# Kernel optimization log

Hardware: AMD Instinct MI355X
Metric: run time of the kernel (lower is better)

Reference implementation:

```python
import jax, jax.numpy as jnp
import numpy as np

INPUT_SIZE = 32
UNITS = 1024
T = 8192
N_MODULES = 2
INPUT_SCALING = 1.0
SPECTRAL_RADIUS = 0.99
LEAKY = 0.5
C_IN = 10
C_REC = 10


def _sparse_input_kernel(rng, M, N, C):
    # each row (input dim) projects to C random reservoir units, U(-1,1)
    W = np.zeros((M, N), dtype=np.float32)
    for i in range(M):
        idx = rng.choice(N, size=C, replace=False)
        W[i, idx] = rng.uniform(-1.0, 1.0, size=C).astype(np.float32)
    return W


def _sparse_recurrent_kernel(rng, M, C):
    # each column (unit) receives input from C random units, U(-1,1)
    W = np.zeros((M, M), dtype=np.float32)
    for i in range(M):
        idx = rng.choice(M, size=C, replace=False)
        W[idx, i] = rng.uniform(-1.0, 1.0, size=C).astype(np.float32)
    return W


def _make_recurrent(rng, M, leaky, rho):
    W = _sparse_recurrent_kernel(rng, M, C_REC)
    I = np.eye(M, dtype=np.float32)
    if leaky == 1:
        e = np.linalg.eigvals(W)
        W = W * (rho / np.max(np.abs(e)))
    else:
        W = W * leaky + I * (1.0 - leaky)
        e = np.linalg.eigvals(W)
        W = W * (rho / np.max(np.abs(e)))
        W = (W + I * (leaky - 1.0)) * (1.0 / leaky)
    return W.astype(np.float32)


def setup_inputs() -> dict:
    key = jax.random.key(0)
    rng = np.random.default_rng(0)
    u = jax.random.normal(key, (1, T, INPUT_SIZE), dtype=jnp.float32)
    # module 0: input_size -> units; module 1: units -> units
    kernel0 = jnp.asarray(_sparse_input_kernel(rng, INPUT_SIZE, UNITS, C_IN) * INPUT_SCALING)
    rec0 = jnp.asarray(_make_recurrent(rng, UNITS, LEAKY, SPECTRAL_RADIUS))
    bias0 = jnp.asarray(rng.uniform(-1.0, 1.0, size=UNITS).astype(np.float32))
    kernel1 = jnp.asarray(_sparse_input_kernel(rng, UNITS, UNITS, C_IN) * INPUT_SCALING)
    rec1 = jnp.asarray(_make_recurrent(rng, UNITS, LEAKY, SPECTRAL_RADIUS))
    bias1 = jnp.asarray(rng.uniform(-1.0, 1.0, size=UNITS).astype(np.float32))
    return {"u": u, "kernel0": kernel0, "rec0": rec0, "bias0": bias0,
            "kernel1": kernel1, "rec1": rec1, "bias1": bias1}


def _run_reservoir(u, K, W, b):
    # u: [B, T, in]; leaky-integrator ESN scan over time
    def step(h, ut):
        out = jnp.tanh(ut @ K + b + h @ W)
        h_new = h * (1.0 - LEAKY) + out * LEAKY
        return h_new, h_new
    h0 = jnp.zeros((u.shape[0], K.shape[1]), dtype=u.dtype)
    _, hs = jax.lax.scan(step, h0, jnp.swapaxes(u, 0, 1))  # [T, B, units]
    return jnp.swapaxes(hs, 0, 1)  # [B, T, units]


def reference(u, kernel0, rec0, bias0, kernel1, rec1, bias1):
    hs0 = _run_reservoir(u, kernel0, rec0, bias0)
    hs1 = _run_reservoir(hs0, kernel1, rec1, bias1)
    # deep reservoir output: concatenation of all module state sequences
    return jnp.concatenate([hs0, hs1], axis=-1)  # [1, T, 2*UNITS]
```

## Files before the change

### kernel.cpp

```cpp
#include <hip/hip_runtime.h>
#include <math.h>

typedef unsigned int uint;

#define T_STEPS 8192
#define R_CAP 10
#define K1_CAP 32
#define K0_CAP 8

__global__ __launch_bounds__(256) void prep_extract(
    const float* __restrict__ k0w, const float* __restrict__ r0w,
    const float* __restrict__ r1w, const float* __restrict__ k1w,
    float* __restrict__ r0vr, uint* __restrict__ r0ur, float* __restrict__ d0r,
    float* __restrict__ r1vr, uint* __restrict__ r1ur, float* __restrict__ d1r,
    float* __restrict__ k1vr, uint* __restrict__ k1ur, int* __restrict__ c1r,
    float* __restrict__ k0vr, uint* __restrict__ k0ur, int* __restrict__ c0r)
{
    int tid = blockIdx.x * 256 + threadIdx.x;
    int task = tid >> 10, j = tid & 1023;

    if (task <= 1) {
        const float* W = task ? r1w : r0w;
        float* vr = task ? r1vr : r0vr;
        uint*  ur = task ? r1ur : r0ur;
        float* dr = task ? d1r  : d0r;
        float diag = 0.f; int c = 0;
#pragma unroll 4
        for (int i = 0; i < 1024; ++i) {
            float v = W[i * 1024 + j];
            if (i == j) diag = v;
            else if (v != 0.f && c < R_CAP) {
                vr[j * R_CAP + c] = v; ur[j * R_CAP + c] = (uint)i; ++c;
            }
        }
        for (; c < R_CAP; ++c) { vr[j * R_CAP + c] = 0.f; ur[j * R_CAP + c] = 0u; }
        dr[j] = diag;
    } else if (task == 2) {
        int c = 0;
#pragma unroll 4
        for (int i = 0; i < 1024; ++i) {
            float v = k1w[i * 1024 + j];
            if (v != 0.f && c < K1_CAP) {
                k1vr[j * K1_CAP + c] = v; k1ur[j * K1_CAP + c] = (uint)i; ++c;
            }
        }
        c1r[j] = c;
        for (int q = c; q < K1_CAP; ++q) { k1vr[j * K1_CAP + q] = 0.f; k1ur[j * K1_CAP + q] = 0u; }
    } else {
        int c = 0;
        for (int i = 0; i < 32; ++i) {
            float v = k0w[i * 1024 + j];
            if (v != 0.f && c < K0_CAP) {
                k0vr[j * K0_CAP + c] = v; k0ur[j * K0_CAP + c] = (uint)i; ++c;
            }
        }
        c0r[j] = c;
        for (int q = c; q < K0_CAP; ++q) { k0vr[j * K0_CAP + q] = 0.f; k0ur[j * K0_CAP + q] = 0u; }
    }
}

__global__ __launch_bounds__(1024) void prep_slots(
    const float* __restrict__ r0vr, const uint* __restrict__ r0ur,
    const float* __restrict__ r1vr, const uint* __restrict__ r1ur,
    const float* __restrict__ k1vr, const uint* __restrict__ k1ur, const int* __restrict__ c1r,
    const float* __restrict__ k0vr, const uint* __restrict__ k0ur, const int* __restrict__ c0r,
    uint* __restrict__ Gr0a, float* __restrict__ Gr0v, int* __restrict__ Gcr0,
    uint* __restrict__ Gr1a, float* __restrict__ Gr1v, int* __restrict__ Gcr1,
    uint* __restrict__ Gk1a, float* __restrict__ Gk1v, int* __restrict__ Fc1,
    uint* __restrict__ Gk0a, float* __restrict__ Gk0v, int* __restrict__ Fc0,
    int* __restrict__ Fu0, int* __restrict__ Fu1,
    int* __restrict__ Linv0, int* __restrict__ Linv1)
{
    __shared__ int lc1[1024], lc0[1024];
    __shared__ unsigned short sl0[1024], sl1[1024];
    const int j = threadIdx.x;
    const int c1j = c1r[j], c0j = c0r[j];
    lc1[j] = c1j; lc0[j] = c0j;
    __syncthreads();
    int s1 = 0, s0 = 0;
#pragma unroll 4
    for (int i = 0; i < 1024; ++i) {
        int a = lc1[i]; s1 += (a < c1j) || (a == c1j && i < j);
        int b = lc0[i]; s0 += (b < c0j) || (b == c0j && i < j);
    }
    sl0[j] = (unsigned short)s0;
    sl1[j] = (unsigned short)s1;
    __syncthreads();

    {
        int n = 0;
        for (int k = 0; k < R_CAP; ++k) {
            float v = r0vr[j * R_CAP + k];
            uint  u = r0ur[j * R_CAP + k];
            Gr0v[s0 * R_CAP + k] = v;
            Gr0a[s0 * R_CAP + k] = (v != 0.f) ? ((uint)sl0[u] << 2) : 0u;
            if (v != 0.f) n = k + 1;
        }
        Gcr0[s0] = n;
        for (int k = 0; k < K0_CAP; ++k) {
            Gk0v[s0 * K0_CAP + k] = k0vr[j * K0_CAP + k];
            Gk0a[s0 * K0_CAP + k] = (k < c0j) ? (k0ur[j * K0_CAP + k] << 2) : 0u;
        }
        Fc0[s0] = c0j; Fu0[s0] = j;
    }
    {
        int n = 0;
        for (int k = 0; k < R_CAP; ++k) {
            float v = r1vr[j * R_CAP + k];
            uint  u = r1ur[j * R_CAP + k];
            Gr1v[s1 * R_CAP + k] = v;
            Gr1a[s1 * R_CAP + k] = (v != 0.f) ? ((uint)sl1[u] << 2) : 0u;
            if (v != 0.f) n = k + 1;
        }
        Gcr1[s1] = n;
        for (int k = 0; k < K1_CAP; ++k) {
            Gk1v[s1 * K1_CAP + k] = k1vr[j * K1_CAP + k];
            Gk1a[s1 * K1_CAP + k] = (k < c1j) ? ((uint)sl0[k1ur[j * K1_CAP + k]] << 2) : 0u;
        }
        Fc1[s1] = c1j; Fu1[s1] = j;
    }
    Linv0[j] = s0;
    Linv1[j] = s1;
}

__global__ __launch_bounds__(256) void prep_greedy(
    const uint* __restrict__ Gr0a, const float* __restrict__ Gr0v, const int* __restrict__ Gcr0,
    const uint* __restrict__ Gr1a, const float* __restrict__ Gr1v, const int* __restrict__ Gcr1,
    const uint* __restrict__ Gk1a, const float* __restrict__ Gk1v, const int* __restrict__ Fc1,
    const uint* __restrict__ Gk0a, const float* __restrict__ Gk0v, const int* __restrict__ Fc0,
    float* __restrict__ Fr0v, uint* __restrict__ Fr0a,
    float* __restrict__ Fr1v, uint* __restrict__ Fr1a,
    float* __restrict__ Fk1v, uint* __restrict__ Fk1a,
    float* __restrict__ Fk0v, uint* __restrict__ Fk0a)
{
    __shared__ uint  ea[4][64][32];
    __shared__ float ev[4][64][32];
    __shared__ int   bl[4][32];
    const int wv   = threadIdx.x >> 6;
    const int lane = threadIdx.x & 63;
    const int gw   = blockIdx.x * 4 + wv;
    const int task = gw >> 4;
    const int col  = (gw & 15) * 64 + lane;

    const uint* ga; const float* gv; const int* gc; int cap;
    float* fv; uint* fa;
    if (task == 0)      { ga = Gr0a; gv = Gr0v; gc = Gcr0; cap = R_CAP;  fv = Fr0v; fa = Fr0a; }
    else if (task == 1) { ga = Gr1a; gv = Gr1v; gc = Gcr1; cap = R_CAP;  fv = Fr1v; fa = Fr1a; }
    else if (task == 2) { ga = Gk1a; gv = Gk1v; gc = Fc1;  cap = K1_CAP; fv = Fk1v; fa = Fk1a; }
    else                { ga = Gk0a; gv = Gk0v; gc = Fc0;  cap = K0_CAP; fv = Fk0v; fa = Fk0a; }

    const int cnt = gc[col];
    for (int s = 0; s < cap; ++s) {
        ea[wv][lane][s] = ga[col * cap + s];
        ev[wv][lane][s] = gv[col * cap + s];
    }
    __syncthreads();

    for (int slot = 0; slot < 32; ++slot) {
        if (lane < 32) bl[wv][lane] = 0;
        __syncthreads();
        int pick = -1;
        const bool active = (slot < cap) && (slot < cnt);
        for (int rnd = 0; rnd < 3; ++rnd) {
            if (active && pick < 0) {
                int best = slot, bload = 1 << 30;
                for (int e = slot; e < cnt; ++e) {
                    int b  = (int)((ea[wv][lane][e] >> 2) & 31u);
                    int ld = bl[wv][b];
                    if (ld < bload) { bload = ld; best = e; }
                }
                int bb = (int)((ea[wv][lane][best] >> 2) & 31u);
                if (rnd == 2) {
                    atomicAdd(&bl[wv][bb], 1); pick = best;
                } else {
                    int old = atomicAdd(&bl[wv][bb], 1);
                    if (old >= 2) atomicSub(&bl[wv][bb], 1);
                    else pick = best;
                }
            }
            __syncthreads();
        }
        if (active && pick > slot) {
            uint  ta = ea[wv][lane][slot]; ea[wv][lane][slot] = ea[wv][lane][pick]; ea[wv][lane][pick] = ta;
            float tv = ev[wv][lane][slot]; ev[wv][lane][slot] = ev[wv][lane][pick]; ev[wv][lane][pick] = tv;
        }
        __syncthreads();
    }

    for (int s = 0; s < cap; ++s) fv[col * cap + s] = ev[wv][lane][s];
    for (int p = 0; p < cap / 2; ++p)
        fa[col * (cap / 2) + p] = (ea[wv][lane][2 * p] & 0xffffu) | (ea[wv][lane][2 * p + 1] << 16);
}

__device__ __forceinline__ float fast_tanh(float x) {
    float ax = fabsf(x);
    float e  = __expf(-2.0f * ax);
    float r  = __builtin_amdgcn_rcpf(1.0f + e);
    float t  = (1.0f - e) * r;
    return copysignf(t, x);
}

#define LD(A) (*(const float*)(smem + (A)))

#define STEP(P, UOFF, DO1)                                                     \
  {                                                                            \
    float xa = __builtin_fmaf(d0, h0j, b0), xb = 0.f;                          \
    _Pragma("unroll")                                                          \
    for (int k = 0; k < R_CAP; k += 2) {                                       \
      uint pr = r0a[k >> 1];                                                   \
      xa += r0v[k]     * LD((pr & 0xffffu) + (P) * 4096);                      \
      xb += r0v[k + 1] * LD((pr >> 16)     + (P) * 4096);                      \
    }                                                                          \
    _Pragma("unroll")                                                          \
    for (int kc = 0; kc < K0_CAP; kc += 2) {                                   \
      if (kc < k0m) {                                                          \
        uint pr = k0a[kc >> 1];                                                \
        xa += k0v[kc]     * LD((pr & 0xffffu) + (UOFF));                       \
        xb += k0v[kc + 1] * LD((pr >> 16)     + (UOFF));                       \
      }                                                                        \
    }                                                                          \
    float o0  = fast_tanh(xa + xb);                                            \
    float h0n = 0.5f * (h0j + o0);                                             \
    ((float*)(smem + (1 - (P)) * 4096))[j] = h0n;                              \
    __syncthreads();                                                           \
    float g0 = LD((uint)l0off + (1 - (P)) * 4096);                             \
    float g1 = 0.f;                                                            \
    if (DO1) g1 = LD(8192u + (uint)l1off + (P) * 4096);                        \
    float ya = __builtin_fmaf(d1, h1j, b1), yb = 0.f;                          \
    _Pragma("unroll")                                                          \
    for (int kc = 0; kc < K1_CAP; kc += 4) {                                   \
      if (kc < k1m) {                                                          \
        uint pa = k1a[kc >> 1], pb = k1a[(kc >> 1) + 1];                       \
        ya += k1v[kc]     * LD((pa & 0xffffu) + (1 - (P)) * 4096);             \
        yb += k1v[kc + 1] * LD((pa >> 16)     + (1 - (P)) * 4096);             \
        ya += k1v[kc + 2] * LD((pb & 0xffffu) + (1 - (P)) * 4096);             \
        yb += k1v[kc + 3] * LD((pb >> 16)     + (1 - (P)) * 4096);             \
      }                                                                        \
    }                                                                          \
    _Pragma("unroll")                                                          \
    for (int k = 0; k < R_CAP; k += 2) {                                       \
      uint pr = r1a[k >> 1];                                                   \
      ya += r1v[k]     * LD((pr & 0xffffu) + 8192u + (P) * 4096);              \
      yb += r1v[k + 1] * LD((pr >> 16)     + 8192u + (P) * 4096);              \
    }                                                                          \
    *o0p = g0; o0p += 2048;                                                    \
    if (DO1) { *o1p = g1; o1p += 2048; }                                       \
    float o1  = fast_tanh(ya + yb);                                            \
    float h1n = 0.5f * (h1j + o1);                                             \
    ((float*)(smem + 8192u + (1 - (P)) * 4096))[j] = h1n;                      \
    h0j = h0n; h1j = h1n;                                                      \
  }

__global__ __launch_bounds__(1024, 4) void reservoir_main(
    const float* __restrict__ u,
    const float* __restrict__ bias0, const float* __restrict__ bias1,
    const float* __restrict__ d0r, const float* __restrict__ d1r,
    const float* __restrict__ Fr0v, const uint* __restrict__ Fr0a,
    const float* __restrict__ Fr1v, const uint* __restrict__ Fr1a,
    const float* __restrict__ Fk1v, const uint* __restrict__ Fk1a,
    const float* __restrict__ Fk0v, const uint* __restrict__ Fk0a,
    const int* __restrict__ Fc1, const int* __restrict__ Fc0,
    const int* __restrict__ Fu0, const int* __restrict__ Fu1,
    const int* __restrict__ Linv0, const int* __restrict__ Linv1,
    float* __restrict__ out)
{
    __shared__ __align__(16) char smem[24576];
    const int j = threadIdx.x;

    float r0v[R_CAP], r1v[R_CAP], k1v[K1_CAP], k0v[K0_CAP];
    uint  r0a[R_CAP / 2], r1a[R_CAP / 2], k1a[K1_CAP / 2], k0a[K0_CAP / 2];
#pragma unroll
    for (int k = 0; k < R_CAP; ++k) { r0v[k] = Fr0v[j * R_CAP + k]; r1v[k] = Fr1v[j * R_CAP + k]; }
#pragma unroll
    for (int k = 0; k < R_CAP / 2; ++k) { r0a[k] = Fr0a[j * (R_CAP / 2) + k]; r1a[k] = Fr1a[j * (R_CAP / 2) + k]; }
#pragma unroll
    for (int k = 0; k < K1_CAP; ++k) k1v[k] = Fk1v[j * K1_CAP + k];
#pragma unroll
    for (int k = 0; k < K1_CAP / 2; ++k) k1a[k] = Fk1a[j * (K1_CAP / 2) + k];
#pragma unroll
    for (int k = 0; k < K0_CAP; ++k) k0v[k] = Fk0v[j * K0_CAP + k];
#pragma unroll
    for (int k = 0; k < K0_CAP / 2; ++k) k0a[k] = Fk0a[j * (K0_CAP / 2) + k];

    const int u0 = Fu0[j], u1 = Fu1[j];
    const float b0 = bias0[u0], d0 = d0r[u0];
    const float b1 = bias1[u1], d1 = d1r[u1];
    const int l0off = Linv0[j] << 2;
    const int l1off = Linv1[j] << 2;
    float* o0p = out + j;
    float* o1p = out + 1024 + j;

    int k1m = Fc1[j], k0m = Fc0[j];
#pragma unroll
    for (int s = 32; s >= 1; s >>= 1) {
        int a = __shfl_xor(k1m, s, 64); k1m = a > k1m ? a : k1m;
        int b = __shfl_xor(k0m, s, 64); k0m = b > k0m ? b : k0m;
    }
    k1m = __builtin_amdgcn_readfirstlane((k1m + 3) & ~3);
    k0m = __builtin_amdgcn_readfirstlane((k0m + 1) & ~1);

    ((float*)(smem        ))[j] = 0.f;
    ((float*)(smem +  4096))[j] = 0.f;
    ((float*)(smem +  8192))[j] = 0.f;
    ((float*)(smem + 12288))[j] = 0.f;
    float h0j = 0.f, h1j = 0.f;

    {
        ((float*)(smem + 16384))[j]        = u[j];
        ((float*)(smem + 16384))[1024 + j] = u[1024 + j];
        __syncthreads();
        STEP(0, 16384u, 0)
        STEP(1, 16384u + 128u, 1)
    }
    for (int t = 2; t < T_STEPS; t += 2) {
        if ((t & 63) == 0) {
            ((float*)(smem + 16384))[j]        = u[t * 32 + j];
            ((float*)(smem + 16384))[1024 + j] = u[t * 32 + 1024 + j];
            __syncthreads();
        }
        uint uoff = 16384u + (uint)((t & 63) << 7);
        STEP(0, uoff, 1)
        STEP(1, uoff + 128u, 1)
    }
    __syncthreads();
    *o1p = LD(8192u + (uint)l1off);
}

extern "C" void kernel_launch(void* const* d_in, const int* in_sizes, int n_in,
                              void* d_out, int out_size, void* d_ws, size_t ws_size,
                              hipStream_t stream) {
    const float* u   = (const float*)d_in[0];
    const float* k0w = (const float*)d_in[1];
    const float* r0w = (const float*)d_in[2];
    const float* b0  = (const float*)d_in[3];
    const float* k1w = (const float*)d_in[4];
    const float* r1w = (const float*)d_in[5];
    const float* b1  = (const float*)d_in[6];
    float* out = (float*)d_out;

    char* w = (char*)d_ws;
    float* r0vr = (float*)w; w += 1024 * R_CAP * 4;
    uint*  r0ur = (uint*)w;  w += 1024 * R_CAP * 4;
    float* d0r  = (float*)w; w += 1024 * 4;
    float* r1vr = (float*)w; w += 1024 * R_CAP * 4;
    uint*  r1ur = (uint*)w;  w += 1024 * R_CAP * 4;
    float* d1r  = (float*)w; w += 1024 * 4;
    float* k1vr = (float*)w; w += 1024 * K1_CAP * 4;
    uint*  k1ur = (uint*)w;  w += 1024 * K1_CAP * 4;
    int*   c1r  = (int*)w;   w += 1024 * 4;
    float* k0vr = (float*)w; w += 1024 * K0_CAP * 4;
    uint*  k0ur = (uint*)w;  w += 1024 * K0_CAP * 4;
    int*   c0r  = (int*)w;   w += 1024 * 4;
    uint*  Gr0a = (uint*)w;  w += 1024 * R_CAP * 4;
    float* Gr0v = (float*)w; w += 1024 * R_CAP * 4;
    int*   Gcr0 = (int*)w;   w += 1024 * 4;
    uint*  Gr1a = (uint*)w;  w += 1024 * R_CAP * 4;
    float* Gr1v = (float*)w; w += 1024 * R_CAP * 4;
    int*   Gcr1 = (int*)w;   w += 1024 * 4;
    uint*  Gk1a = (uint*)w;  w += 1024 * K1_CAP * 4;
    float* Gk1v = (float*)w; w += 1024 * K1_CAP * 4;
    uint*  Gk0a = (uint*)w;  w += 1024 * K0_CAP * 4;
    float* Gk0v = (float*)w; w += 1024 * K0_CAP * 4;
    float* Fr0v = (float*)w; w += 1024 * R_CAP * 4;
    uint*  Fr0a = (uint*)w;  w += 1024 * (R_CAP / 2) * 4;
    float* Fr1v = (float*)w; w += 1024 * R_CAP * 4;
    uint*  Fr1a = (uint*)w;  w += 1024 * (R_CAP / 2) * 4;
    float* Fk1v = (float*)w; w += 1024 * K1_CAP * 4;
    uint*  Fk1a = (uint*)w;  w += 1024 * (K1_CAP / 2) * 4;
    float* Fk0v = (float*)w; w += 1024 * K0_CAP * 4;
    uint*  Fk0a = (uint*)w;  w += 1024 * (K0_CAP / 2) * 4;
    int*   Fc1  = (int*)w;   w += 1024 * 4;
    int*   Fc0  = (int*)w;   w += 1024 * 4;
    int*   Fu0  = (int*)w;   w += 1024 * 4;
    int*   Fu1  = (int*)w;   w += 1024 * 4;
    int*   Linv0 = (int*)w;  w += 1024 * 4;
    int*   Linv1 = (int*)w;

    prep_extract<<<16, 256, 0, stream>>>(k0w, r0w, r1w, k1w,
                                         r0vr, r0ur, d0r, r1vr, r1ur, d1r,
                                         k1vr, k1ur, c1r, k0vr, k0ur, c0r);
    prep_slots<<<1, 1024, 0, stream>>>(r0vr, r0ur, r1vr, r1ur,
                                       k1vr, k1ur, c1r, k0vr, k0ur, c0r,
                                       Gr0a, Gr0v, Gcr0, Gr1a, Gr1v, Gcr1,
                                       Gk1a, Gk1v, Fc1, Gk0a, Gk0v, Fc0,
                                       Fu0, Fu1, Linv0, Linv1);
    prep_greedy<<<16, 256, 0, stream>>>(Gr0a, Gr0v, Gcr0, Gr1a, Gr1v, Gcr1,
                                        Gk1a, Gk1v, Fc1, Gk0a, Gk0v, Fc0,
                                        Fr0v, Fr0a, Fr1v, Fr1a,
                                        Fk1v, Fk1a, Fk0v, Fk0a);
    reservoir_main<<<1, 1024, 0, stream>>>(u, b0, b1, d0r, d1r,
                                           Fr0v, Fr0a, Fr1v, Fr1a,
                                           Fk1v, Fk1a, Fk0v, Fk0a,
                                           Fc1, Fc0, Fu0, Fu1, Linv0, Linv1,
                                           out);
}
```

Baseline: 17.85 ms.

## Keep module-0 units in natural order and tighten LDS bank balancing

Module-0 units are no longer sorted by input count, so each thread owns unit j directly. This lets the layer-0 output be written straight to global memory without an extra shared-memory gather, and removes the Fu0/Linv0 indirection. The greedy slot assignment now balances LDS banks per half-wave with stricter occupancy and an extra round. The gathers use four accumulators instead of two for more ILP, and the K0 cap drops from 8 to 6. The cap of 6 assumes no input row-to-unit mapping gives a unit more than 6 inputs, and module-0 warps may diverge more on input counts.

Measured after the change: 15.85 ms. 1.13x faster.

```diff
diff --git a/kernel.cpp b/kernel.cpp
--- a/kernel.cpp
+++ b/kernel.cpp
@@ -6,7 +6,7 @@
 #define T_STEPS 8192
 #define R_CAP 10
 #define K1_CAP 32
-#define K0_CAP 8
+#define K0_CAP 6
 
 __global__ __launch_bounds__(256) void prep_extract(
     const float* __restrict__ k0w, const float* __restrict__ r0w,
@@ -68,22 +68,19 @@
     uint* __restrict__ Gr1a, float* __restrict__ Gr1v, int* __restrict__ Gcr1,
     uint* __restrict__ Gk1a, float* __restrict__ Gk1v, int* __restrict__ Fc1,
     uint* __restrict__ Gk0a, float* __restrict__ Gk0v, int* __restrict__ Fc0,
-    int* __restrict__ Fu0, int* __restrict__ Fu1,
-    int* __restrict__ Linv0, int* __restrict__ Linv1)
+    int* __restrict__ Fu1, int* __restrict__ Linv1)
 {
-    __shared__ int lc1[1024], lc0[1024];
-    __shared__ unsigned short sl0[1024], sl1[1024];
+    __shared__ int lc1[1024];
+    __shared__ unsigned short sl1[1024];
     const int j = threadIdx.x;
     const int c1j = c1r[j], c0j = c0r[j];
-    lc1[j] = c1j; lc0[j] = c0j;
+    lc1[j] = c1j;
     __syncthreads();
-    int s1 = 0, s0 = 0;
+    int s1 = 0;
 #pragma unroll 4
     for (int i = 0; i < 1024; ++i) {
         int a = lc1[i]; s1 += (a < c1j) || (a == c1j && i < j);
-        int b = lc0[i]; s0 += (b < c0j) || (b == c0j && i < j);
-    }
-    sl0[j] = (unsigned short)s0;
+    }
     sl1[j] = (unsigned short)s1;
     __syncthreads();
 
@@ -92,16 +89,16 @@
         for (int k = 0; k < R_CAP; ++k) {
             float v = r0vr[j * R_CAP + k];
             uint  u = r0ur[j * R_CAP + k];
-            Gr0v[s0 * R_CAP + k] = v;
-            Gr0a[s0 * R_CAP + k] = (v != 0.f) ? ((uint)sl0[u] << 2) : 0u;
+            Gr0v[j * R_CAP + k] = v;
+            Gr0a[j * R_CAP + k] = (v != 0.f) ? (u << 2) : 0u;
             if (v != 0.f) n = k + 1;
         }
-        Gcr0[s0] = n;
+        Gcr0[j] = n;
         for (int k = 0; k < K0_CAP; ++k) {
-            Gk0v[s0 * K0_CAP + k] = k0vr[j * K0_CAP + k];
-            Gk0a[s0 * K0_CAP + k] = (k < c0j) ? (k0ur[j * K0_CAP + k] << 2) : 0u;
-        }
-        Fc0[s0] = c0j; Fu0[s0] = j;
+            Gk0v[j * K0_CAP + k] = k0vr[j * K0_CAP + k];
+            Gk0a[j * K0_CAP + k] = (k < c0j) ? (k0ur[j * K0_CAP + k] << 2) : 0u;
+        }
+        Fc0[j] = c0j;
     }
     {
         int n = 0;
@@ -109,17 +106,16 @@
             float v = r1vr[j * R_CAP + k];
             uint  u = r1ur[j * R_CAP + k];
             Gr1v[s1 * R_CAP + k] = v;
-            Gr1a[s1 * R_CAP + k] = (v != 0.f) ? ((uint)sl1[u] << 2) : 0u;
+            Gr1a[s1 * R_CAP + k] = (v != 0.f) ? (8192u + ((uint)sl1[u] << 2)) : 8192u;
             if (v != 0.f) n = k + 1;
         }
         Gcr1[s1] = n;
         for (int k = 0; k < K1_CAP; ++k) {
             Gk1v[s1 * K1_CAP + k] = k1vr[j * K1_CAP + k];
-            Gk1a[s1 * K1_CAP + k] = (k < c1j) ? ((uint)sl0[k1ur[j * K1_CAP + k]] << 2) : 0u;
+            Gk1a[s1 * K1_CAP + k] = (k < c1j) ? (k1ur[j * K1_CAP + k] << 2) : 0u;
         }
         Fc1[s1] = c1j; Fu1[s1] = j;
     }
-    Linv0[j] = s0;
     Linv1[j] = s1;
 }
 
@@ -135,9 +131,10 @@
 {
     __shared__ uint  ea[4][64][32];
     __shared__ float ev[4][64][32];
-    __shared__ int   bl[4][32];
+    __shared__ int   bl[4][64];
     const int wv   = threadIdx.x >> 6;
     const int lane = threadIdx.x & 63;
+    const int half = (lane >> 5) * 32;
     const int gw   = blockIdx.x * 4 + wv;
     const int task = gw >> 4;
     const int col  = (gw & 15) * 64 + lane;
@@ -157,24 +154,24 @@
     __syncthreads();
 
     for (int slot = 0; slot < 32; ++slot) {
-        if (lane < 32) bl[wv][lane] = 0;
+        bl[wv][lane] = 0;
         __syncthreads();
         int pick = -1;
         const bool active = (slot < cap) && (slot < cnt);
-        for (int rnd = 0; rnd < 3; ++rnd) {
+        for (int rnd = 0; rnd < 4; ++rnd) {
             if (active && pick < 0) {
                 int best = slot, bload = 1 << 30;
                 for (int e = slot; e < cnt; ++e) {
                     int b  = (int)((ea[wv][lane][e] >> 2) & 31u);
-                    int ld = bl[wv][b];
+                    int ld = bl[wv][half + b];
                     if (ld < bload) { bload = ld; best = e; }
                 }
                 int bb = (int)((ea[wv][lane][best] >> 2) & 31u);
-                if (rnd == 2) {
-                    atomicAdd(&bl[wv][bb], 1); pick = best;
+                if (rnd == 3) {
+                    atomicAdd(&bl[wv][half + bb], 1); pick = best;
                 } else {
-                    int old = atomicAdd(&bl[wv][bb], 1);
-                    if (old >= 2) atomicSub(&bl[wv][bb], 1);
+                    int old = atomicAdd(&bl[wv][half + bb], 1);
+                    if (old >= 1) atomicSub(&bl[wv][half + bb], 1);
                     else pick = best;
                 }
             }
@@ -204,50 +201,63 @@
 
 #define STEP(P, UOFF, DO1)                                                     \
   {                                                                            \
-    float xa = __builtin_fmaf(d0, h0j, b0), xb = 0.f;                          \
-    _Pragma("unroll")                                                          \
-    for (int k = 0; k < R_CAP; k += 2) {                                       \
-      uint pr = r0a[k >> 1];                                                   \
-      xa += r0v[k]     * LD((pr & 0xffffu) + (P) * 4096);                      \
-      xb += r0v[k + 1] * LD((pr >> 16)     + (P) * 4096);                      \
+    float xa = __builtin_fmaf(d0, h0j, b0), xb = 0.f, xc = 0.f, xd = 0.f;      \
+    {                                                                          \
+      uint p0 = r0a[0], p1 = r0a[1], p2 = r0a[2], p3 = r0a[3], p4 = r0a[4];    \
+      xa += r0v[0] * LD((p0 & 0xffffu) + (P) * 4096u);                         \
+      xb += r0v[1] * LD((p0 >> 16)     + (P) * 4096u);                         \
+      xc += r0v[2] * LD((p1 & 0xffffu) + (P) * 4096u);                         \
+      xd += r0v[3] * LD((p1 >> 16)     + (P) * 4096u);                         \
+      xa += r0v[4] * LD((p2 & 0xffffu) + (P) * 4096u);                         \
+      xb += r0v[5] * LD((p2 >> 16)     + (P) * 4096u);                         \
+      xc += r0v[6] * LD((p3 & 0xffffu) + (P) * 4096u);                         \
+      xd += r0v[7] * LD((p3 >> 16)     + (P) * 4096u);                         \
+      xa += r0v[8] * LD((p4 & 0xffffu) + (P) * 4096u);                         \
+      xb += r0v[9] * LD((p4 >> 16)     + (P) * 4096u);                         \
     }                                                                          \
     _Pragma("unroll")                                                          \
     for (int kc = 0; kc < K0_CAP; kc += 2) {                                   \
       if (kc < k0m) {                                                          \
         uint pr = k0a[kc >> 1];                                                \
-        xa += k0v[kc]     * LD((pr & 0xffffu) + (UOFF));                       \
-        xb += k0v[kc + 1] * LD((pr >> 16)     + (UOFF));                       \
+        xc += k0v[kc]     * LD((pr & 0xffffu) + (UOFF));                       \
+        xd += k0v[kc + 1] * LD((pr >> 16)     + (UOFF));                       \
       }                                                                        \
     }                                                                          \
-    float o0  = fast_tanh(xa + xb);                                            \
+    float o0  = fast_tanh((xa + xb) + (xc + xd));                              \
     float h0n = 0.5f * (h0j + o0);                                             \
-    ((float*)(smem + (1 - (P)) * 4096))[j] = h0n;                              \
+    ((float*)(smem + (1 - (P)) * 4096u))[j] = h0n;                             \
+    *o0p = h0n; o0p += 2048;                                                   \
     __syncthreads();                                                           \
-    float g0 = LD((uint)l0off + (1 - (P)) * 4096);                             \
     float g1 = 0.f;                                                            \
-    if (DO1) g1 = LD(8192u + (uint)l1off + (P) * 4096);                        \
-    float ya = __builtin_fmaf(d1, h1j, b1), yb = 0.f;                          \
+    if (DO1) g1 = LD(8192u + (P) * 4096u + l1off);                             \
+    float ya = __builtin_fmaf(d1, h1j, b1), yb = 0.f, yc = 0.f, yd = 0.f;      \
     _Pragma("unroll")                                                          \
     for (int kc = 0; kc < K1_CAP; kc += 4) {                                   \
       if (kc < k1m) {                                                          \
         uint pa = k1a[kc >> 1], pb = k1a[(kc >> 1) + 1];                       \
-        ya += k1v[kc]     * LD((pa & 0xffffu) + (1 - (P)) * 4096);             \
-        yb += k1v[kc + 1] * LD((pa >> 16)     + (1 - (P)) * 4096);             \
-        ya += k1v[kc + 2] * LD((pb & 0xffffu) + (1 - (P)) * 4096);             \
-        yb += k1v[kc + 3] * LD((pb >> 16)     + (1 - (P)) * 4096);             \
+        ya += k1v[kc]     * LD((pa & 0xffffu) + (1 - (P)) * 4096u);            \
+        yb += k1v[kc + 1] * LD((pa >> 16)     + (1 - (P)) * 4096u);            \
+        yc += k1v[kc + 2] * LD((pb & 0xffffu) + (1 - (P)) * 4096u);            \
+        yd += k1v[kc + 3] * LD((pb >> 16)     + (1 - (P)) * 4096u);            \
       }                                                                        \
     }                                                                          \
-    _Pragma("unroll")                                                          \
-    for (int k = 0; k < R_CAP; k += 2) {                                       \
-      uint pr = r1a[k >> 1];                                                   \
-      ya += r1v[k]     * LD((pr & 0xffffu) + 8192u + (P) * 4096);              \
-      yb += r1v[k + 1] * LD((pr >> 16)     + 8192u + (P) * 4096);              \
+    {                                                                          \
+      uint p0 = r1a[0], p1 = r1a[1], p2 = r1a[2], p3 = r1a[3], p4 = r1a[4];    \
+      ya += r1v[0] * LD((p0 & 0xffffu) + (P) * 4096u);                         \
+      yb += r1v[1] * LD((p0 >> 16)     + (P) * 4096u);                         \
+      yc += r1v[2] * LD((p1 & 0xffffu) + (P) * 4096u);                         \
+      yd += r1v[3] * LD((p1 >> 16)     + (P) * 4096u);                         \
+      ya += r1v[4] * LD((p2 & 0xffffu) + (P) * 4096u);                         \
+      yb += r1v[5] * LD((p2 >> 16)     + (P) * 4096u);                         \
+      yc += r1v[6] * LD((p3 & 0xffffu) + (P) * 4096u);                         \
+      yd += r1v[7] * LD((p3 >> 16)     + (P) * 4096u);                         \
+      ya += r1v[8] * LD((p4 & 0xffffu) + (P) * 4096u);                         \
+      yb += r1v[9] * LD((p4 >> 16)     + (P) * 4096u);                         \
     }                                                                          \
-    *o0p = g0; o0p += 2048;                                                    \
     if (DO1) { *o1p = g1; o1p += 2048; }                                       \
-    float o1  = fast_tanh(ya + yb);                                            \
+    float o1  = fast_tanh((ya + yb) + (yc + yd));                              \
     float h1n = 0.5f * (h1j + o1);                                             \
-    ((float*)(smem + 8192u + (1 - (P)) * 4096))[j] = h1n;                      \
+    ((float*)(smem + 8192u + (1 - (P)) * 4096u))[j] = h1n;                     \
     h0j = h0n; h1j = h1n;                                                      \
   }
 
@@ -260,8 +270,7 @@
     const float* __restrict__ Fk1v, const uint* __restrict__ Fk1a,
     const float* __restrict__ Fk0v, const uint* __restrict__ Fk0a,
     const int* __restrict__ Fc1, const int* __restrict__ Fc0,
-    const int* __restrict__ Fu0, const int* __restrict__ Fu1,
-    const int* __restrict__ Linv0, const int* __restrict__ Linv1,
+    const int* __restrict__ Fu1, const int* __restrict__ Linv1,
     float* __restrict__ out)
 {
     __shared__ __align__(16) char smem[24576];
@@ -282,11 +291,10 @@
 #pragma unroll
     for (int k = 0; k < K0_CAP / 2; ++k) k0a[k] = Fk0a[j * (K0_CAP / 2) + k];
 
-    const int u0 = Fu0[j], u1 = Fu1[j];
-    const float b0 = bias0[u0], d0 = d0r[u0];
+    const int u1 = Fu1[j];
+    const float b0 = bias0[j],  d0 = d0r[j];
     const float b1 = bias1[u1], d1 = d1r[u1];
-    const int l0off = Linv0[j] << 2;
-    const int l1off = Linv1[j] << 2;
+    const uint l1off = (uint)(Linv1[j] << 2);
     float* o0p = out + j;
     float* o1p = out + 1024 + j;
 
@@ -323,7 +331,7 @@
         STEP(1, uoff + 128u, 1)
     }
     __syncthreads();
-    *o1p = LD(8192u + (uint)l1off);
+    *o1p = LD(8192u + l1off);
 }
 
 extern "C" void kernel_launch(void* const* d_in, const int* in_sizes, int n_in,
@@ -371,9 +379,7 @@
     uint*  Fk0a = (uint*)w;  w += 1024 * (K0_CAP / 2) * 4;
     int*   Fc1  = (int*)w;   w += 1024 * 4;
     int*   Fc0  = (int*)w;   w += 1024 * 4;
-    int*   Fu0  = (int*)w;   w += 1024 * 4;
     int*   Fu1  = (int*)w;   w += 1024 * 4;
-    int*   Linv0 = (int*)w;  w += 1024 * 4;
     int*   Linv1 = (int*)w;
 
     prep_extract<<<16, 256, 0, stream>>>(k0w, r0w, r1w, k1w,
@@ -383,7 +389,7 @@
                                        k1vr, k1ur, c1r, k0vr, k0ur, c0r,
                                        Gr0a, Gr0v, Gcr0, Gr1a, Gr1v, Gcr1,
                                        Gk1a, Gk1v, Fc1, Gk0a, Gk0v, Fc0,
-                                       Fu0, Fu1, Linv0, Linv1);
+                                       Fu1, Linv1);
     prep_greedy<<<16, 256, 0, stream>>>(Gr0a, Gr0v, Gcr0, Gr1a, Gr1v, Gcr1,
                                         Gk1a, Gk1v, Fc1, Gk0a, Gk0v, Fc0,
                                         Fr0v, Fr0a, Fr1v, Fr1a,
@@ -391,6 +397,6 @@
     reservoir_main<<<1, 1024, 0, stream>>>(u, b0, b1, d0r, d1r,
                                            Fr0v, Fr0a, Fr1v, Fr1a,
                                            Fk1v, Fk1a, Fk0v, Fk0a,
-                                           Fc1, Fc0, Fu0, Fu1, Linv0, Linv1,
+                                           Fc1, Fc0, Fu1, Linv1,
                                            out);
 }
```
